# Kernel optimization log

Hardware: AMD Instinct MI355X
Metric: run time of the kernel (lower is better)

## Reference

```python
import jax, jax.numpy as jnp
import numpy as np
import math

B, S, DM, H, DQK, DV, L = 2, 1024, 1024, 16, 64, 64, 32


def setup_inputs() -> dict:
    key = jax.random.key(0)
    ks = jax.random.split(key, 16)
    sdm = 1.0 / np.sqrt(DM)
    u = lambda k, shape, s: jax.random.uniform(k, shape, jnp.float32, -s, s)
    return {
        "q_in": jax.random.normal(ks[0], (B, S, DM), jnp.float32),
        "k_in": jax.random.normal(ks[1], (B, S, DM), jnp.float32),
        "v_in": jax.random.normal(ks[2], (B, S, DM), jnp.float32),
        "attn_mask": jnp.zeros((B, S, S), jnp.bool_),
        "q_pos_ids": jnp.tile(jnp.arange(S, dtype=jnp.int32)[None, :], (B, 1)),
        "kv_pos_ids": jnp.tile(jnp.arange(S, dtype=jnp.int32)[None, :], (B, 1)),
        "W_q": u(ks[3], (H * DQK, DM), sdm),
        "b_q": u(ks[4], (H * DQK,), sdm),
        "W_k": u(ks[5], (H * DQK, DM), sdm),
        "b_k": u(ks[6], (H * DQK,), sdm),
        "W_v": u(ks[7], (H * DV, DM), sdm),
        "b_v": u(ks[8], (H * DV,), sdm),
        "W_o": u(ks[9], (DM, H * DV), sdm),
        "b_o": u(ks[10], (DM,), sdm),
        "W_rel": u(ks[11], (2 * L + 1, DQK), 1.0 / np.sqrt(DQK)),
        "talking_w": u(ks[12], (H, H), 1.0 / np.sqrt(H)),
    }


def reference(q_in, k_in, v_in, attn_mask, q_pos_ids, kv_pos_ids,
              W_q, b_q, W_k, b_k, W_v, b_v, W_o, b_o, W_rel, talking_w):
    Bq, Q, _ = q_in.shape
    # projections + head split
    q = (q_in @ W_q.T + b_q).reshape(Bq, Q, H, DQK)   # [B,Q,H,dqk]
    k = (k_in @ W_k.T + b_k).reshape(Bq, -1, H, DQK)  # [B,K,H,dqk]
    v = (v_in @ W_v.T + b_v).reshape(Bq, -1, H, DV)   # [B,K,H,dv]

    rel = q_pos_ids[:, :, None] - kv_pos_ids[:, None, :]  # [B,Q,K]
    idx = jnp.clip(rel, -L, L) + L
    pos_key = W_rel[idx]            # [B,Q,K,dqk]
    pos_value = pos_key             # original forward reuses rel_pos_k_emb for values

    # alibi slopes: start * ratio**i with ratio == start
    start = 2.0 ** (-2.0 ** (-(math.log2(H) - 3)))
    slopes = jnp.asarray([start * start ** i for i in range(H)], q.dtype)
    alibi = jnp.abs(rel).astype(q.dtype)[:, None, :, :] * slopes[None, :, None, None]

    scores = jnp.einsum('bqnd,bknd->bnqk', q, k)
    scores = scores + jnp.einsum('bqnd,bqkd->bnqk', q, pos_key)
    scores = scores + alibi
    scores = jnp.einsum('bnqk,nm->bmqk', scores, talking_w)  # talking heads
    scores = scores / jnp.sqrt(jnp.asarray(DQK, q.dtype))
    scores = jnp.where(attn_mask[:, None, :, :], jnp.asarray(-10000.0, q.dtype), scores)
    attn = jax.nn.softmax(scores, axis=-1)

    out = jnp.einsum('bnqk,bknd->bnqd', attn, v)
    out = out + jnp.einsum('bnqk,bqkd->bnqd', attn, pos_value)
    out = out.transpose(0, 2, 1, 3).reshape(Bq, Q, H * DV)
    out = out @ W_o.T + b_o
    return (out, attn, scores)
```

## Files before the change

### kernel.cpp

```cpp
#include <hip/hip_runtime.h>

constexpr int kS = 1024;

__global__ __launch_bounds__(256) void gemm_nt(
    const float* __restrict__ A, const float* __restrict__ Bm,
    const float* __restrict__ bias, float* __restrict__ C,
    int K, int lda, int ldb, int ldc,
    long sAo, long sAi, long sBo, long sBi, long sC)
{
    __shared__ float As[32][132];
    __shared__ float Bs[32][132];
    const int t = threadIdx.x;
    const int z = blockIdx.z;
    const long offA = (long)(z >> 4) * sAo + (long)(z & 15) * sAi;
    const long offB = (long)(z >> 4) * sBo + (long)(z & 15) * sBi;
    const long offC = (long)z * sC;
    const int m0 = blockIdx.y * 128;
    const int n0 = blockIdx.x * 128;
    const int sr = t >> 3;
    const int sc = (t & 7) << 2;
    const int tx = t & 15, ty = t >> 4;

    float acc[8][8];
#pragma unroll
    for (int i = 0; i < 8; ++i)
#pragma unroll
        for (int j = 0; j < 8; ++j) acc[i][j] = 0.f;

    for (int k0 = 0; k0 < K; k0 += 32) {
#pragma unroll
        for (int r = 0; r < 4; ++r) {
            const int m = sr + 32 * r;
            const float4 av = *(const float4*)&A[offA + (long)(m0 + m) * lda + k0 + sc];
            As[sc + 0][m] = av.x; As[sc + 1][m] = av.y;
            As[sc + 2][m] = av.z; As[sc + 3][m] = av.w;
            const float4 bv = *(const float4*)&Bm[offB + (long)(n0 + m) * ldb + k0 + sc];
            Bs[sc + 0][m] = bv.x; Bs[sc + 1][m] = bv.y;
            Bs[sc + 2][m] = bv.z; Bs[sc + 3][m] = bv.w;
        }
        __syncthreads();
#pragma unroll 4
        for (int kk = 0; kk < 32; ++kk) {
            float a8[8], b8[8];
            *(float4*)&a8[0] = *(const float4*)&As[kk][ty * 8];
            *(float4*)&a8[4] = *(const float4*)&As[kk][ty * 8 + 4];
            *(float4*)&b8[0] = *(const float4*)&Bs[kk][tx * 8];
            *(float4*)&b8[4] = *(const float4*)&Bs[kk][tx * 8 + 4];
#pragma unroll
            for (int i = 0; i < 8; ++i)
#pragma unroll
                for (int j = 0; j < 8; ++j)
                    acc[i][j] = fmaf(a8[i], b8[j], acc[i][j]);
        }
        __syncthreads();
    }

    float bv[8];
#pragma unroll
    for (int j = 0; j < 8; ++j) bv[j] = bias ? bias[n0 + tx * 8 + j] : 0.f;
#pragma unroll
    for (int i = 0; i < 8; ++i) {
        float o[8];
#pragma unroll
        for (int j = 0; j < 8; ++j) o[j] = acc[i][j] + bv[j];
        float* cp = &C[offC + (long)(m0 + ty * 8 + i) * ldc + n0 + tx * 8];
        *(float4*)&cp[0] = *(const float4*)&o[0];
        *(float4*)&cp[4] = *(const float4*)&o[4];
    }
}

__global__ __launch_bounds__(256) void qrel2_kernel(
    const float* __restrict__ qproj, const float* __restrict__ W_rel,
    const float* __restrict__ tw, float* __restrict__ qrel2)
{
    __shared__ float qrow[1024];
    __shared__ float wrT[64 * 66];
    __shared__ float twl[256];
    __shared__ float qr[16 * 65];
    const int t = threadIdx.x;
    const long bs = blockIdx.x;
    const float* qp = qproj + bs * 1024;
    for (int i = t; i < 1024; i += 256) qrow[i] = qp[i];
    for (int i = t; i < 65 * 64; i += 256) {
        const int j = i >> 6, d = i & 63;
        wrT[d * 66 + j] = W_rel[i];
    }
    twl[t] = tw[t];
    __syncthreads();
    for (int p = t; p < 16 * 65; p += 256) {
        const int n = p / 65, j = p % 65;
        float s = 0.f;
#pragma unroll 8
        for (int d = 0; d < 64; ++d) s = fmaf(qrow[n * 64 + d], wrT[d * 66 + j], s);
        qr[n * 65 + j] = s;
    }
    __syncthreads();
    for (int p = t; p < 16 * 65; p += 256) {
        const int m = p / 65, j = p % 65;
        float s = 0.f;
#pragma unroll
        for (int n = 0; n < 16; ++n) s = fmaf(twl[n * 16 + m], qr[n * 65 + j], s);
        qrel2[bs * (16 * 65) + p] = s;
    }
}

__global__ __launch_bounds__(256) void mix_kernel(
    float* __restrict__ scores, const float* __restrict__ qrel2,
    const float* __restrict__ tw, const unsigned char* __restrict__ mask,
    const int* __restrict__ qpos, const int* __restrict__ kpos,
    float* __restrict__ statp)
{
    __shared__ float qr2[16 * 65];
    __shared__ float twl[256];
    __shared__ float cm[16];
    __shared__ float redm[4][16];
    __shared__ float reds[4][16];
    __shared__ float gmax[16];
    const int t = threadIdx.x;
    const int kc = blockIdx.x;
    const int q = blockIdx.y;
    const int b = blockIdx.z;
    const int k = kc * 256 + t;

    const float* q2p = qrel2 + (long)(b * kS + q) * (16 * 65);
    for (int i = t; i < 16 * 65; i += 256) qr2[i] = q2p[i];
    twl[t] = tw[t];
    __syncthreads();
    if (t < 16) {
        float s = 0.f, cur = 0.7071067811865476f;
        for (int n = 0; n < 16; ++n) { s = fmaf(cur, twl[n * 16 + t], s); cur *= 0.7071067811865476f; }
        cm[t] = s;
    }
    __syncthreads();

    const int rel = qpos[b * kS + q] - kpos[b * kS + k];
    const int idxc = (rel < -32 ? -32 : (rel > 32 ? 32 : rel)) + 32;
    const float ab = fabsf((float)rel);
    const bool msk = mask[((long)b * kS + q) * kS + k] != 0;

    float pre[16];
#pragma unroll
    for (int n = 0; n < 16; ++n)
        pre[n] = scores[((long)(b * 16 + n) * kS + q) * kS + k];
    float sm[16];
#pragma unroll
    for (int m = 0; m < 16; ++m) sm[m] = 0.f;
#pragma unroll
    for (int n = 0; n < 16; ++n) {
        const float p = pre[n];
#pragma unroll
        for (int m = 0; m < 16; ++m) sm[m] = fmaf(p, twl[n * 16 + m], sm[m]);
    }
#pragma unroll
    for (int m = 0; m < 16; ++m) {
        float v = (sm[m] + qr2[m * 65 + idxc] + ab * cm[m]) * 0.125f;
        v = msk ? -10000.f : v;
        sm[m] = v;
        scores[((long)(b * 16 + m) * kS + q) * kS + k] = v;
    }

    const int lane = t & 63, wv = t >> 6;
    float mx[16];
#pragma unroll
    for (int m = 0; m < 16; ++m) mx[m] = sm[m];
#pragma unroll
    for (int m = 0; m < 16; ++m)
        for (int d = 1; d < 64; d <<= 1)
            mx[m] = fmaxf(mx[m], __shfl_xor(mx[m], d, 64));
    if (lane == 0)
        for (int m = 0; m < 16; ++m) redm[wv][m] = mx[m];
    __syncthreads();
    if (t < 16) {
        float v = redm[0][t];
        for (int w = 1; w < 4; ++w) v = fmaxf(v, redm[w][t]);
        gmax[t] = v;
    }
    __syncthreads();
    float sx[16];
#pragma unroll
    for (int m = 0; m < 16; ++m) sx[m] = expf(sm[m] - gmax[m]);
#pragma unroll
    for (int m = 0; m < 16; ++m)
        for (int d = 1; d < 64; d <<= 1)
            sx[m] += __shfl_xor(sx[m], d, 64);
    if (lane == 0)
        for (int m = 0; m < 16; ++m) reds[wv][m] = sx[m];
    __syncthreads();
    if (t < 16) {
        const float l = reds[0][t] + reds[1][t] + reds[2][t] + reds[3][t];
        float2* sp = (float2*)statp;
        sp[((long)(b * 16 + t) * kS + q) * 4 + kc] = make_float2(gmax[t], l);
    }
}

__global__ __launch_bounds__(256) void stats_final(
    const float* __restrict__ statp, float* __restrict__ stats)
{
    const int r = blockIdx.x * 256 + threadIdx.x;
    const float* p = statp + (long)r * 8;
    float M = -1e30f;
#pragma unroll
    for (int i = 0; i < 4; ++i) M = fmaxf(M, p[i * 2]);
    float l = 0.f;
#pragma unroll
    for (int i = 0; i < 4; ++i) l += p[i * 2 + 1] * expf(p[i * 2] - M);
    l = fmaxf(l, 1e-30f);
    stats[r * 2] = M;
    stats[r * 2 + 1] = 1.f / l;
}

__global__ __launch_bounds__(256) void attn_pv(
    const float* __restrict__ scores, float* __restrict__ attn,
    const float* __restrict__ vproj, const float* __restrict__ wrel_g,
    const float* __restrict__ stats, float* __restrict__ head_out)
{
    __shared__ float atT[64][68];
    __shared__ float vs[64][64];
    __shared__ float amid[64][64];
    __shared__ float red_lo[64][16];
    __shared__ float red_hi[64][16];
    __shared__ float MR[64][2];
    __shared__ float wrl[65 * 64];

    const int t = threadIdx.x;
    const int q0 = blockIdx.x * 64;
    const int h = blockIdx.y;
    const int b = blockIdx.z;

    if (t < 64) {
        const float2 s2 = ((const float2*)stats)[(long)(b * 16 + h) * kS + q0 + t];
        MR[t][0] = s2.x; MR[t][1] = s2.y;
    }
    for (int i = t; i < 65 * 64; i += 256) wrl[i] = wrel_g[i];
    {
        float* amf = &amid[0][0];
        for (int i = t; i < 64 * 64; i += 256) amf[i] = 0.f;
    }

    const int g = t >> 7;
    const int u = t & 127;
    const int txd = u & 15, tyq = u >> 4;
    const int qs = tyq * 8, ds = txd * 4;
    const int korg = g * 32;
    const int arow = t >> 4;
    const int akq = (t & 15) * 4;

    float acc[8][4];
#pragma unroll
    for (int i = 0; i < 8; ++i)
#pragma unroll
        for (int j = 0; j < 4; ++j) acc[i][j] = 0.f;
    float slo[4] = {0.f, 0.f, 0.f, 0.f};
    float shi[4] = {0.f, 0.f, 0.f, 0.f};

    const long scb = (long)(b * 16 + h) * kS;
    for (int kt = 0; kt < 16; ++kt) {
        const int k0 = kt * 64;
        __syncthreads();
#pragma unroll
        for (int r = 0; r < 4; ++r) {
            const int krow = arow + 16 * r;
            const float4 vv = *(const float4*)&vproj[(((long)(b * kS + k0 + krow)) * 16 + h) * 64 + akq];
            *(float4*)&vs[krow][akq] = vv;
        }
#pragma unroll
        for (int r = 0; r < 4; ++r) {
            const int qrow = arow + 16 * r;
            const int qg = q0 + qrow;
            const long off = (scb + qg) * kS + k0 + akq;
            const float4 s4 = *(const float4*)&scores[off];
            const float M = MR[qrow][0], R = MR[qrow][1];
            const float a0 = expf(s4.x - M) * R;
            const float a1 = expf(s4.y - M) * R;
            const float a2 = expf(s4.z - M) * R;
            const float a3 = expf(s4.w - M) * R;
            const float4 a4o = make_float4(a0, a1, a2, a3);
            *(float4*)&attn[off] = a4o;
            atT[akq + 0][qrow] = a0;
            atT[akq + 1][qrow] = a1;
            atT[akq + 2][qrow] = a2;
            atT[akq + 3][qrow] = a3;
            const float av[4] = {a0, a1, a2, a3};
#pragma unroll
            for (int j = 0; j < 4; ++j) {
                const int kg = k0 + akq + j;
                const int jj = qg - kg + 32;
                if (jj >= 1 && jj <= 63) amid[qrow][jj] = av[j];
                else if (jj >= 64) slo[r] += av[j];
                else shi[r] += av[j];
            }
        }
        __syncthreads();
#pragma unroll 4
        for (int kk = 0; kk < 32; ++kk) {
            const int k = korg + kk;
            float a8[8], v4[4];
            *(float4*)&a8[0] = *(const float4*)&atT[k][qs];
            *(float4*)&a8[4] = *(const float4*)&atT[k][qs + 4];
            *(float4*)&v4[0] = *(const float4*)&vs[k][ds];
#pragma unroll
            for (int i = 0; i < 8; ++i)
#pragma unroll
                for (int j = 0; j < 4; ++j)
                    acc[i][j] = fmaf(a8[i], v4[j], acc[i][j]);
        }
    }
    __syncthreads();
    float* pvp = &vs[0][0];
    if (g == 1) {
#pragma unroll
        for (int i = 0; i < 8; ++i)
#pragma unroll
            for (int j = 0; j < 4; ++j) pvp[u * 32 + i * 4 + j] = acc[i][j];
    }
#pragma unroll
    for (int r = 0; r < 4; ++r) {
        const int qrow = arow + 16 * r;
        red_lo[qrow][t & 15] = slo[r];
        red_hi[qrow][t & 15] = shi[r];
    }
    __syncthreads();
    if (g == 0) {
#pragma unroll
        for (int i = 0; i < 8; ++i)
#pragma unroll
            for (int j = 0; j < 4; ++j) acc[i][j] += pvp[u * 32 + i * 4 + j];
#pragma unroll
        for (int i = 0; i < 8; ++i) {
            const int qrow = qs + i;
            float Sl = 0.f, Sh = 0.f;
#pragma unroll
            for (int l = 0; l < 16; ++l) { Sl += red_lo[qrow][l]; Sh += red_hi[qrow][l]; }
#pragma unroll
            for (int j = 0; j < 4; ++j)
                acc[i][j] += Sh * wrl[ds + j] + Sl * wrl[64 * 64 + ds + j];
        }
        for (int jj = 1; jj < 64; ++jj) {
            float wv[4];
            *(float4*)&wv[0] = *(const float4*)&wrl[jj * 64 + ds];
#pragma unroll
            for (int i = 0; i < 8; ++i) {
                const float am = amid[qs + i][jj];
#pragma unroll
                for (int j = 0; j < 4; ++j) acc[i][j] = fmaf(am, wv[j], acc[i][j]);
            }
        }
#pragma unroll
        for (int i = 0; i < 8; ++i) {
            float* op = &head_out[(((long)(b * kS + q0 + qs + i)) * 16 + h) * 64 + ds];
            *(float4*)&op[0] = *(const float4*)&acc[i][0];
        }
    }
}

extern "C" void kernel_launch(void* const* d_in, const int* in_sizes, int n_in,
                              void* d_out, int out_size, void* d_ws, size_t ws_size,
                              hipStream_t stream)
{
    const float* q_in = (const float*)d_in[0];
    const float* k_in = (const float*)d_in[1];
    const float* v_in = (const float*)d_in[2];
    const unsigned char* mask = (const unsigned char*)d_in[3];
    const int* qpos = (const int*)d_in[4];
    const int* kpos = (const int*)d_in[5];
    const float* W_q = (const float*)d_in[6];
    const float* b_q = (const float*)d_in[7];
    const float* W_k = (const float*)d_in[8];
    const float* b_k = (const float*)d_in[9];
    const float* W_v = (const float*)d_in[10];
    const float* b_v = (const float*)d_in[11];
    const float* W_o = (const float*)d_in[12];
    const float* b_o = (const float*)d_in[13];
    const float* W_rel = (const float*)d_in[14];
    const float* tw = (const float*)d_in[15];

    float* ws = (float*)d_ws;
    float* qb = ws;
    float* kb = qb + 2097152;
    float* vb = kb + 2097152;
    float* q2 = vb + 2097152;
    float* statp = q2 + 2129920;
    float* stats = statp + 262144;
    float* hout = stats + 65536;

    float* out = (float*)d_out;
    float* attn = out + 2097152;
    float* scores = attn + 33554432;

    const dim3 blk(256, 1, 1);
    const dim3 gp(8, 16, 1);
    gemm_nt<<<gp, blk, 0, stream>>>(q_in, W_q, b_q, qb, 1024, 1024, 1024, 1024, 0L, 0L, 0L, 0L, 0L);
    gemm_nt<<<gp, blk, 0, stream>>>(k_in, W_k, b_k, kb, 1024, 1024, 1024, 1024, 0L, 0L, 0L, 0L, 0L);
    gemm_nt<<<gp, blk, 0, stream>>>(v_in, W_v, b_v, vb, 1024, 1024, 1024, 1024, 0L, 0L, 0L, 0L, 0L);
    qrel2_kernel<<<dim3(2048, 1, 1), blk, 0, stream>>>(qb, W_rel, tw, q2);
    const dim3 gpre(8, 8, 32);
    gemm_nt<<<gpre, blk, 0, stream>>>(qb, kb, (const float*)nullptr, scores,
                                      64, 1024, 1024, 1024,
                                      1048576L, 64L, 1048576L, 64L, 1048576L);
    const dim3 gmix(4, 1024, 2);
    mix_kernel<<<gmix, blk, 0, stream>>>(scores, q2, tw, mask, qpos, kpos, statp);
    stats_final<<<dim3(128, 1, 1), blk, 0, stream>>>(statp, stats);
    const dim3 gk4(16, 16, 2);
    attn_pv<<<gk4, blk, 0, stream>>>(scores, attn, vb, W_rel, stats, hout);
    gemm_nt<<<gp, blk, 0, stream>>>(hout, W_o, b_o, out, 1024, 1024, 1024, 1024, 0L, 0L, 0L, 0L, 0L);
}
```

Before: 1.163 ms.

## Move projections and QK scores to bf16 MFMA and fuse QK with head mixing

Inputs and weights are converted to bf16, and all four projection GEMMs now run on MFMA 16x16x32 bf16 instructions with XOR-swizzled LDS tiles. The Q, K and V projections are batched into one launch. The separate QK^T GEMM and mix kernel are fused into a qkmix kernel. It computes per-head QK on MFMA, applies talking-heads mixing in registers, and produces per-block softmax partial stats. This avoids writing pre-mix scores to global memory and reading them back. V and the head output are kept in bf16, which reduces precision and adds conversion kernels.

After: 1.556 ms. 1.34x slower.

```diff
diff --git a/kernel.cpp b/kernel.cpp
--- a/kernel.cpp
+++ b/kernel.cpp
@@ -2,76 +2,119 @@
 
 constexpr int kS = 1024;
 
-__global__ __launch_bounds__(256) void gemm_nt(
-    const float* __restrict__ A, const float* __restrict__ Bm,
-    const float* __restrict__ bias, float* __restrict__ C,
-    int K, int lda, int ldb, int ldc,
-    long sAo, long sAi, long sBo, long sBi, long sC)
-{
-    __shared__ float As[32][132];
-    __shared__ float Bs[32][132];
+typedef __attribute__((ext_vector_type(8))) short s16x8;
+typedef __attribute__((ext_vector_type(4))) float f32x4;
+
+__device__ __forceinline__ unsigned short f2bf(float x) {
+    unsigned int u = __float_as_uint(x);
+    u += 0x7FFFu + ((u >> 16) & 1u);
+    return (unsigned short)(u >> 16);
+}
+__device__ __forceinline__ float bf2f(unsigned short h) {
+    return __uint_as_float(((unsigned int)h) << 16);
+}
+
+__global__ __launch_bounds__(256) void cvt_multi(
+    const float* __restrict__ s0, const float* __restrict__ s1,
+    const float* __restrict__ s2, const float* __restrict__ s3,
+    unsigned short* __restrict__ d0, unsigned short* __restrict__ d1,
+    unsigned short* __restrict__ d2, unsigned short* __restrict__ d3, int n)
+{
+    const int z = blockIdx.y;
+    const float* s = z == 0 ? s0 : z == 1 ? s1 : z == 2 ? s2 : s3;
+    unsigned short* d = z == 0 ? d0 : z == 1 ? d1 : z == 2 ? d2 : d3;
+    const int i = (blockIdx.x * 256 + threadIdx.x) * 8;
+    if (i >= n) return;
+    const float4 a = *(const float4*)&s[i];
+    const float4 b = *(const float4*)&s[i + 4];
+    uint4 st;
+    st.x = (unsigned int)f2bf(a.x) | ((unsigned int)f2bf(a.y) << 16);
+    st.y = (unsigned int)f2bf(a.z) | ((unsigned int)f2bf(a.w) << 16);
+    st.z = (unsigned int)f2bf(b.x) | ((unsigned int)f2bf(b.y) << 16);
+    st.w = (unsigned int)f2bf(b.z) | ((unsigned int)f2bf(b.w) << 16);
+    *(uint4*)&d[i] = st;
+}
+
+__global__ __launch_bounds__(256, 2) void gemm_bf16(
+    const unsigned short* __restrict__ A, const unsigned short* __restrict__ B,
+    const float* __restrict__ bi0, const float* __restrict__ bi1, const float* __restrict__ bi2,
+    float* __restrict__ Cf, unsigned short* __restrict__ Cb,
+    int K, int N, long sA, long sB, long sC)
+{
+    __shared__ __align__(16) unsigned short As[128 * 64];
+    __shared__ __align__(16) unsigned short Bs[128 * 64];
     const int t = threadIdx.x;
     const int z = blockIdx.z;
-    const long offA = (long)(z >> 4) * sAo + (long)(z & 15) * sAi;
-    const long offB = (long)(z >> 4) * sBo + (long)(z & 15) * sBi;
-    const long offC = (long)z * sC;
-    const int m0 = blockIdx.y * 128;
-    const int n0 = blockIdx.x * 128;
-    const int sr = t >> 3;
-    const int sc = (t & 7) << 2;
-    const int tx = t & 15, ty = t >> 4;
-
-    float acc[8][8];
-#pragma unroll
-    for (int i = 0; i < 8; ++i)
-#pragma unroll
-        for (int j = 0; j < 8; ++j) acc[i][j] = 0.f;
-
-    for (int k0 = 0; k0 < K; k0 += 32) {
-#pragma unroll
-        for (int r = 0; r < 4; ++r) {
-            const int m = sr + 32 * r;
-            const float4 av = *(const float4*)&A[offA + (long)(m0 + m) * lda + k0 + sc];
-            As[sc + 0][m] = av.x; As[sc + 1][m] = av.y;
-            As[sc + 2][m] = av.z; As[sc + 3][m] = av.w;
-            const float4 bv = *(const float4*)&Bm[offB + (long)(n0 + m) * ldb + k0 + sc];
-            Bs[sc + 0][m] = bv.x; Bs[sc + 1][m] = bv.y;
-            Bs[sc + 2][m] = bv.z; Bs[sc + 3][m] = bv.w;
-        }
-        __syncthreads();
-#pragma unroll 4
-        for (int kk = 0; kk < 32; ++kk) {
-            float a8[8], b8[8];
-            *(float4*)&a8[0] = *(const float4*)&As[kk][ty * 8];
-            *(float4*)&a8[4] = *(const float4*)&As[kk][ty * 8 + 4];
-            *(float4*)&b8[0] = *(const float4*)&Bs[kk][tx * 8];
-            *(float4*)&b8[4] = *(const float4*)&Bs[kk][tx * 8 + 4];
-#pragma unroll
-            for (int i = 0; i < 8; ++i)
-#pragma unroll
-                for (int j = 0; j < 8; ++j)
-                    acc[i][j] = fmaf(a8[i], b8[j], acc[i][j]);
-        }
-        __syncthreads();
-    }
-
-    float bv[8];
-#pragma unroll
-    for (int j = 0; j < 8; ++j) bv[j] = bias ? bias[n0 + tx * 8 + j] : 0.f;
-#pragma unroll
-    for (int i = 0; i < 8; ++i) {
-        float o[8];
-#pragma unroll
-        for (int j = 0; j < 8; ++j) o[j] = acc[i][j] + bv[j];
-        float* cp = &C[offC + (long)(m0 + ty * 8 + i) * ldc + n0 + tx * 8];
-        *(float4*)&cp[0] = *(const float4*)&o[0];
-        *(float4*)&cp[4] = *(const float4*)&o[4];
-    }
+    const float* bi = (z == 0) ? bi0 : ((z == 1) ? bi1 : bi2);
+    const int n0 = blockIdx.x * 128, m0 = blockIdx.y * 128;
+    const int w = t >> 6, l = t & 63;
+    const int wm = w >> 1, wn = w & 1;
+    const long Ab = (long)z * sA, Bb = (long)z * sB, Cbse = (long)z * sC;
+
+    f32x4 acc[4][4];
+#pragma unroll
+    for (int i = 0; i < 4; ++i)
+#pragma unroll
+        for (int j = 0; j < 4; ++j) acc[i][j] = (f32x4){0.f, 0.f, 0.f, 0.f};
+
+    for (int k0 = 0; k0 < K; k0 += 64) {
+#pragma unroll
+        for (int i = 0; i < 4; ++i) {
+            const int p = i * 256 + t;
+            const int r = p >> 3, slot = p & 7;
+            const int ck = slot ^ (r & 7);
+            const s16x8 av = *(const s16x8*)&A[Ab + (long)(m0 + r) * K + k0 + ck * 8];
+            const s16x8 bv = *(const s16x8*)&B[Bb + (long)(n0 + r) * K + k0 + ck * 8];
+            *(s16x8*)&As[p * 8] = av;
+            *(s16x8*)&Bs[p * 8] = bv;
+        }
+        __syncthreads();
+#pragma unroll
+        for (int s = 0; s < 2; ++s) {
+            s16x8 af[4], bfr[4];
+            const int g = l >> 4;
+            const int ck = s * 4 + g;
+#pragma unroll
+            for (int mf = 0; mf < 4; ++mf) {
+                const int row = wm * 64 + mf * 16 + (l & 15);
+                af[mf] = *(const s16x8*)&As[(row * 8 + (ck ^ (row & 7))) * 8];
+            }
+#pragma unroll
+            for (int nf = 0; nf < 4; ++nf) {
+                const int col = wn * 64 + nf * 16 + (l & 15);
+                bfr[nf] = *(const s16x8*)&Bs[(col * 8 + (ck ^ (col & 7))) * 8];
+            }
+#pragma unroll
+            for (int mf = 0; mf < 4; ++mf)
+#pragma unroll
+                for (int nf = 0; nf < 4; ++nf)
+                    acc[mf][nf] = __builtin_amdgcn_mfma_f32_16x16x32_bf16(
+                        af[mf], bfr[nf], acc[mf][nf], 0, 0, 0);
+        }
+        __syncthreads();
+    }
+
+    float bv[4];
+#pragma unroll
+    for (int nf = 0; nf < 4; ++nf) bv[nf] = bi ? bi[n0 + wn * 64 + nf * 16 + (l & 15)] : 0.f;
+#pragma unroll
+    for (int mf = 0; mf < 4; ++mf)
+#pragma unroll
+        for (int r2 = 0; r2 < 4; ++r2) {
+            const int row = m0 + wm * 64 + mf * 16 + (l >> 4) * 4 + r2;
+#pragma unroll
+            for (int nf = 0; nf < 4; ++nf) {
+                const int col = n0 + wn * 64 + nf * 16 + (l & 15);
+                const float v = acc[mf][nf][r2] + bv[nf];
+                if (Cf) Cf[Cbse + (long)row * N + col] = v;
+                if (Cb) Cb[Cbse + (long)row * N + col] = f2bf(v);
+            }
+        }
 }
 
 __global__ __launch_bounds__(256) void qrel2_kernel(
-    const float* __restrict__ qproj, const float* __restrict__ W_rel,
-    const float* __restrict__ tw, float* __restrict__ qrel2)
+    const unsigned short* __restrict__ qproj, const float* __restrict__ W_rel,
+    const float* __restrict__ tw, float* __restrict__ qrel2T)
 {
     __shared__ float qrow[1024];
     __shared__ float wrT[64 * 66];
@@ -79,8 +122,13 @@
     __shared__ float qr[16 * 65];
     const int t = threadIdx.x;
     const long bs = blockIdx.x;
-    const float* qp = qproj + bs * 1024;
-    for (int i = t; i < 1024; i += 256) qrow[i] = qp[i];
+    {
+        const ushort4 qv = *(const ushort4*)&qproj[bs * 1024 + t * 4];
+        qrow[t * 4 + 0] = bf2f(qv.x);
+        qrow[t * 4 + 1] = bf2f(qv.y);
+        qrow[t * 4 + 2] = bf2f(qv.z);
+        qrow[t * 4 + 3] = bf2f(qv.w);
+    }
     for (int i = t; i < 65 * 64; i += 256) {
         const int j = i >> 6, d = i & 63;
         wrT[d * 66 + j] = W_rel[i];
@@ -100,119 +148,144 @@
         float s = 0.f;
 #pragma unroll
         for (int n = 0; n < 16; ++n) s = fmaf(twl[n * 16 + m], qr[n * 65 + j], s);
-        qrel2[bs * (16 * 65) + p] = s;
-    }
-}
-
-__global__ __launch_bounds__(256) void mix_kernel(
-    float* __restrict__ scores, const float* __restrict__ qrel2,
-    const float* __restrict__ tw, const unsigned char* __restrict__ mask,
+        qrel2T[bs * 1040 + j * 16 + m] = s;
+    }
+}
+
+__global__ __launch_bounds__(256, 2) void qkmix(
+    const unsigned short* __restrict__ qbp, const unsigned short* __restrict__ kbp,
+    const float* __restrict__ qrel2T, const float* __restrict__ tw,
+    const unsigned char* __restrict__ mask,
     const int* __restrict__ qpos, const int* __restrict__ kpos,
-    float* __restrict__ statp)
-{
-    __shared__ float qr2[16 * 65];
+    float* __restrict__ scores, float2* __restrict__ statp)
+{
+    __shared__ __align__(16) unsigned short qls[32 * 64 * 8];
+    __shared__ __align__(16) unsigned short kls[32 * 64 * 8];
     __shared__ float twl[256];
-    __shared__ float cm[16];
-    __shared__ float redm[4][16];
-    __shared__ float reds[4][16];
-    __shared__ float gmax[16];
+    __shared__ float cmL[16];
+    __shared__ int qposs[32], kposs[32];
+    __shared__ float2 statL[2][32][16];
     const int t = threadIdx.x;
-    const int kc = blockIdx.x;
-    const int q = blockIdx.y;
-    const int b = blockIdx.z;
-    const int k = kc * 256 + t;
-
-    const float* q2p = qrel2 + (long)(b * kS + q) * (16 * 65);
-    for (int i = t; i < 16 * 65; i += 256) qr2[i] = q2p[i];
+    const int k0 = blockIdx.x * 32, q0 = blockIdx.y * 32, b = blockIdx.z;
+    const int w = t >> 6, l = t & 63;
+    const int qoff = (w >> 1) * 16, koff = (w & 1) * 16;
+
     twl[t] = tw[t];
+    if (t < 32) qposs[t] = qpos[b * kS + q0 + t];
+    if (t >= 64 && t < 96) kposs[t - 64] = kpos[b * kS + (t - 64) + k0];
     __syncthreads();
     if (t < 16) {
-        float s = 0.f, cur = 0.7071067811865476f;
-        for (int n = 0; n < 16; ++n) { s = fmaf(cur, twl[n * 16 + t], s); cur *= 0.7071067811865476f; }
-        cm[t] = s;
-    }
-    __syncthreads();
-
-    const int rel = qpos[b * kS + q] - kpos[b * kS + k];
-    const int idxc = (rel < -32 ? -32 : (rel > 32 ? 32 : rel)) + 32;
-    const float ab = fabsf((float)rel);
-    const bool msk = mask[((long)b * kS + q) * kS + k] != 0;
-
-    float pre[16];
-#pragma unroll
-    for (int n = 0; n < 16; ++n)
-        pre[n] = scores[((long)(b * 16 + n) * kS + q) * kS + k];
-    float sm[16];
-#pragma unroll
-    for (int m = 0; m < 16; ++m) sm[m] = 0.f;
-#pragma unroll
-    for (int n = 0; n < 16; ++n) {
-        const float p = pre[n];
-#pragma unroll
-        for (int m = 0; m < 16; ++m) sm[m] = fmaf(p, twl[n * 16 + m], sm[m]);
-    }
-#pragma unroll
-    for (int m = 0; m < 16; ++m) {
-        float v = (sm[m] + qr2[m * 65 + idxc] + ab * cm[m]) * 0.125f;
-        v = msk ? -10000.f : v;
-        sm[m] = v;
-        scores[((long)(b * 16 + m) * kS + q) * kS + k] = v;
-    }
-
-    const int lane = t & 63, wv = t >> 6;
-    float mx[16];
-#pragma unroll
-    for (int m = 0; m < 16; ++m) mx[m] = sm[m];
-#pragma unroll
-    for (int m = 0; m < 16; ++m)
-        for (int d = 1; d < 64; d <<= 1)
-            mx[m] = fmaxf(mx[m], __shfl_xor(mx[m], d, 64));
-    if (lane == 0)
-        for (int m = 0; m < 16; ++m) redm[wv][m] = mx[m];
-    __syncthreads();
-    if (t < 16) {
-        float v = redm[0][t];
-        for (int w = 1; w < 4; ++w) v = fmaxf(v, redm[w][t]);
-        gmax[t] = v;
-    }
-    __syncthreads();
-    float sx[16];
-#pragma unroll
-    for (int m = 0; m < 16; ++m) sx[m] = expf(sm[m] - gmax[m]);
-#pragma unroll
-    for (int m = 0; m < 16; ++m)
-        for (int d = 1; d < 64; d <<= 1)
-            sx[m] += __shfl_xor(sx[m], d, 64);
-    if (lane == 0)
-        for (int m = 0; m < 16; ++m) reds[wv][m] = sx[m];
-    __syncthreads();
-    if (t < 16) {
-        const float l = reds[0][t] + reds[1][t] + reds[2][t] + reds[3][t];
-        float2* sp = (float2*)statp;
-        sp[((long)(b * 16 + t) * kS + q) * 4 + kc] = make_float2(gmax[t], l);
+        float s = 0.f, cur = 0.70710678118654752f;
+        for (int n = 0; n < 16; ++n) { s = fmaf(cur, twl[n * 16 + t], s); cur *= 0.70710678118654752f; }
+        cmL[t] = s;
+    }
+
+    f32x4 acc[16];
+#pragma unroll
+    for (int n = 0; n < 16; ++n) acc[n] = (f32x4){0.f, 0.f, 0.f, 0.f};
+
+#pragma unroll
+    for (int pass = 0; pass < 2; ++pass) {
+        __syncthreads();
+#pragma unroll
+        for (int i = 0; i < 8; ++i) {
+            const int p = i * 256 + t;
+            const int r = p >> 6, slot = p & 63;
+            const int nd = slot ^ (r & 7);
+            *(s16x8*)&qls[p * 8] =
+                *(const s16x8*)&qbp[((long)(b * kS + q0 + r)) * 1024 + pass * 512 + nd * 8];
+            *(s16x8*)&kls[p * 8] =
+                *(const s16x8*)&kbp[((long)(b * kS + k0 + r)) * 1024 + pass * 512 + nd * 8];
+        }
+        __syncthreads();
+#pragma unroll
+        for (int nl = 0; nl < 8; ++nl) {
+            const int g = l >> 4;
+            const int row = qoff + (l & 15);
+            const int col = koff + (l & 15);
+            const s16x8 a0 = *(const s16x8*)&qls[(row * 64 + ((nl * 8 + g) ^ (row & 7))) * 8];
+            const s16x8 a1 = *(const s16x8*)&qls[(row * 64 + ((nl * 8 + 4 + g) ^ (row & 7))) * 8];
+            const s16x8 b0 = *(const s16x8*)&kls[(col * 64 + ((nl * 8 + g) ^ (col & 7))) * 8];
+            const s16x8 b1 = *(const s16x8*)&kls[(col * 64 + ((nl * 8 + 4 + g) ^ (col & 7))) * 8];
+            acc[pass * 8 + nl] = __builtin_amdgcn_mfma_f32_16x16x32_bf16(a0, b0, acc[pass * 8 + nl], 0, 0, 0);
+            acc[pass * 8 + nl] = __builtin_amdgcn_mfma_f32_16x16x32_bf16(a1, b1, acc[pass * 8 + nl], 0, 0, 0);
+        }
+    }
+
+    const int g = l >> 4, cl = l & 15;
+    const int kg_loc = koff + cl;
+    const int kp = kposs[kg_loc];
+    const int kgl = k0 + kg_loc;
+#pragma unroll
+    for (int r = 0; r < 4; ++r) {
+        const int row_l = qoff + g * 4 + r;
+        const int row_g = q0 + row_l;
+        const int rel = qposs[row_l] - kp;
+        const int idx = (rel < -32 ? -32 : (rel > 32 ? 32 : rel)) + 32;
+        const float ab = fabsf((float)rel);
+        const bool msk = mask[((long)b * kS + row_g) * kS + kgl] != 0;
+        const float* q2p = &qrel2T[((long)(b * kS + row_g) * 65 + idx) * 16];
+        float q2v[16];
+        *(float4*)&q2v[0] = *(const float4*)&q2p[0];
+        *(float4*)&q2v[4] = *(const float4*)&q2p[4];
+        *(float4*)&q2v[8] = *(const float4*)&q2p[8];
+        *(float4*)&q2v[12] = *(const float4*)&q2p[12];
+        float val[16];
+#pragma unroll
+        for (int m = 0; m < 16; ++m) {
+            float s = 0.f;
+#pragma unroll
+            for (int n = 0; n < 16; ++n) s = fmaf(acc[n][r], twl[n * 16 + m], s);
+            float v = (s + q2v[m] + ab * cmL[m]) * 0.125f;
+            val[m] = msk ? -10000.f : v;
+            scores[((long)(b * 16 + m) * kS + row_g) * kS + kgl] = val[m];
+        }
+        float smx = 0.f, ssm = 0.f;
+#pragma unroll
+        for (int m = 0; m < 16; ++m) {
+            float mx = val[m];
+            mx = fmaxf(mx, __shfl_xor(mx, 1, 16));
+            mx = fmaxf(mx, __shfl_xor(mx, 2, 16));
+            mx = fmaxf(mx, __shfl_xor(mx, 4, 16));
+            mx = fmaxf(mx, __shfl_xor(mx, 8, 16));
+            float e = __expf(val[m] - mx);
+            e += __shfl_xor(e, 1, 16);
+            e += __shfl_xor(e, 2, 16);
+            e += __shfl_xor(e, 4, 16);
+            e += __shfl_xor(e, 8, 16);
+            if (cl == m) { smx = mx; ssm = e; }
+        }
+        statL[w & 1][row_l][cl] = make_float2(smx, ssm);
+    }
+    __syncthreads();
+    for (int e = t; e < 512; e += 256) {
+        const int row = e >> 4, m = e & 15;
+        const float2 s0 = statL[0][row][m], s1 = statL[1][row][m];
+        const float M = fmaxf(s0.x, s1.x);
+        const float sm = s0.y * __expf(s0.x - M) + s1.y * __expf(s1.x - M);
+        statp[((long)(b * 16 + m) * kS + q0 + row) * 32 + blockIdx.x] = make_float2(M, sm);
     }
 }
 
 __global__ __launch_bounds__(256) void stats_final(
-    const float* __restrict__ statp, float* __restrict__ stats)
-{
-    const int r = blockIdx.x * 256 + threadIdx.x;
-    const float* p = statp + (long)r * 8;
+    const float2* __restrict__ statp, float2* __restrict__ stats)
+{
+    const int rr = blockIdx.x * 256 + threadIdx.x;
+    const float2* p = statp + (long)rr * 32;
     float M = -1e30f;
-#pragma unroll
-    for (int i = 0; i < 4; ++i) M = fmaxf(M, p[i * 2]);
+#pragma unroll 8
+    for (int i = 0; i < 32; ++i) M = fmaxf(M, p[i].x);
     float l = 0.f;
-#pragma unroll
-    for (int i = 0; i < 4; ++i) l += p[i * 2 + 1] * expf(p[i * 2] - M);
+#pragma unroll 8
+    for (int i = 0; i < 32; ++i) l += p[i].y * __expf(p[i].x - M);
     l = fmaxf(l, 1e-30f);
-    stats[r * 2] = M;
-    stats[r * 2 + 1] = 1.f / l;
+    stats[rr] = make_float2(M, 1.f / l);
 }
 
 __global__ __launch_bounds__(256) void attn_pv(
     const float* __restrict__ scores, float* __restrict__ attn,
-    const float* __restrict__ vproj, const float* __restrict__ wrel_g,
-    const float* __restrict__ stats, float* __restrict__ head_out)
+    const unsigned short* __restrict__ vproj, const float* __restrict__ wrel_g,
+    const float2* __restrict__ stats, unsigned short* __restrict__ head_out)
 {
     __shared__ float atT[64][68];
     __shared__ float vs[64][64];
@@ -228,7 +301,7 @@
     const int b = blockIdx.z;
 
     if (t < 64) {
-        const float2 s2 = ((const float2*)stats)[(long)(b * 16 + h) * kS + q0 + t];
+        const float2 s2 = stats[(long)(b * 16 + h) * kS + q0 + t];
         MR[t][0] = s2.x; MR[t][1] = s2.y;
     }
     for (int i = t; i < 65 * 64; i += 256) wrl[i] = wrel_g[i];
@@ -260,8 +333,11 @@
 #pragma unroll
         for (int r = 0; r < 4; ++r) {
             const int krow = arow + 16 * r;
-            const float4 vv = *(const float4*)&vproj[(((long)(b * kS + k0 + krow)) * 16 + h) * 64 + akq];
-            *(float4*)&vs[krow][akq] = vv;
+            const ushort4 vv = *(const ushort4*)&vproj[(((long)(b * kS + k0 + krow)) * 16 + h) * 64 + akq];
+            vs[krow][akq + 0] = bf2f(vv.x);
+            vs[krow][akq + 1] = bf2f(vv.y);
+            vs[krow][akq + 2] = bf2f(vv.z);
+            vs[krow][akq + 3] = bf2f(vv.w);
         }
 #pragma unroll
         for (int r = 0; r < 4; ++r) {
@@ -330,7 +406,7 @@
             const int qrow = qs + i;
             float Sl = 0.f, Sh = 0.f;
 #pragma unroll
-            for (int l = 0; l < 16; ++l) { Sl += red_lo[qrow][l]; Sh += red_hi[qrow][l]; }
+            for (int lq = 0; lq < 16; ++lq) { Sl += red_lo[qrow][lq]; Sh += red_hi[qrow][lq]; }
 #pragma unroll
             for (int j = 0; j < 4; ++j)
                 acc[i][j] += Sh * wrl[ds + j] + Sl * wrl[64 * 64 + ds + j];
@@ -347,8 +423,10 @@
         }
 #pragma unroll
         for (int i = 0; i < 8; ++i) {
-            float* op = &head_out[(((long)(b * kS + q0 + qs + i)) * 16 + h) * 64 + ds];
-            *(float4*)&op[0] = *(const float4*)&acc[i][0];
+            ushort4 h4;
+            h4.x = f2bf(acc[i][0]); h4.y = f2bf(acc[i][1]);
+            h4.z = f2bf(acc[i][2]); h4.w = f2bf(acc[i][3]);
+            *(ushort4*)&head_out[(((long)(b * kS + q0 + qs + i)) * 16 + h) * 64 + ds] = h4;
         }
     }
 }
@@ -374,33 +452,32 @@
     const float* W_rel = (const float*)d_in[14];
     const float* tw = (const float*)d_in[15];
 
-    float* ws = (float*)d_ws;
-    float* qb = ws;
-    float* kb = qb + 2097152;
-    float* vb = kb + 2097152;
-    float* q2 = vb + 2097152;
-    float* statp = q2 + 2129920;
-    float* stats = statp + 262144;
-    float* hout = stats + 65536;
+    unsigned char* W = (unsigned char*)d_ws;
+    unsigned short* in_bf  = (unsigned short*)W;
+    unsigned short* w_bf   = (unsigned short*)(W + 12582912);
+    unsigned short* qkv_bf = (unsigned short*)(W + 20971520);
+    float*          qrel2T = (float*)(W + 33554432);
+    float2*         statp  = (float2*)W;
+    float2*         stats  = (float2*)(W + 42074112);
+    unsigned short* hout   = (unsigned short*)(W + 42336256);
 
     float* out = (float*)d_out;
     float* attn = out + 2097152;
     float* scores = attn + 33554432;
 
     const dim3 blk(256, 1, 1);
-    const dim3 gp(8, 16, 1);
-    gemm_nt<<<gp, blk, 0, stream>>>(q_in, W_q, b_q, qb, 1024, 1024, 1024, 1024, 0L, 0L, 0L, 0L, 0L);
-    gemm_nt<<<gp, blk, 0, stream>>>(k_in, W_k, b_k, kb, 1024, 1024, 1024, 1024, 0L, 0L, 0L, 0L, 0L);
-    gemm_nt<<<gp, blk, 0, stream>>>(v_in, W_v, b_v, vb, 1024, 1024, 1024, 1024, 0L, 0L, 0L, 0L, 0L);
-    qrel2_kernel<<<dim3(2048, 1, 1), blk, 0, stream>>>(qb, W_rel, tw, q2);
-    const dim3 gpre(8, 8, 32);
-    gemm_nt<<<gpre, blk, 0, stream>>>(qb, kb, (const float*)nullptr, scores,
-                                      64, 1024, 1024, 1024,
-                                      1048576L, 64L, 1048576L, 64L, 1048576L);
-    const dim3 gmix(4, 1024, 2);
-    mix_kernel<<<gmix, blk, 0, stream>>>(scores, q2, tw, mask, qpos, kpos, statp);
+    cvt_multi<<<dim3(1024, 3), blk, 0, stream>>>(q_in, k_in, v_in, nullptr,
+        in_bf, in_bf + 2097152, in_bf + 4194304, nullptr, 2097152);
+    cvt_multi<<<dim3(512, 4), blk, 0, stream>>>(W_q, W_k, W_v, W_o,
+        w_bf, w_bf + 1048576, w_bf + 2097152, w_bf + 3145728, 1048576);
+    gemm_bf16<<<dim3(8, 16, 3), blk, 0, stream>>>(in_bf, w_bf, b_q, b_k, b_v,
+        nullptr, qkv_bf, 1024, 1024, 2097152L, 1048576L, 2097152L);
+    qrel2_kernel<<<dim3(2048, 1, 1), blk, 0, stream>>>(qkv_bf, W_rel, tw, qrel2T);
+    qkmix<<<dim3(32, 32, 2), blk, 0, stream>>>(qkv_bf, qkv_bf + 2097152,
+        qrel2T, tw, mask, qpos, kpos, scores, statp);
     stats_final<<<dim3(128, 1, 1), blk, 0, stream>>>(statp, stats);
-    const dim3 gk4(16, 16, 2);
-    attn_pv<<<gk4, blk, 0, stream>>>(scores, attn, vb, W_rel, stats, hout);
-    gemm_nt<<<gp, blk, 0, stream>>>(hout, W_o, b_o, out, 1024, 1024, 1024, 1024, 0L, 0L, 0L, 0L, 0L);
-}
+    attn_pv<<<dim3(16, 16, 2), blk, 0, stream>>>(scores, attn,
+        qkv_bf + 4194304, W_rel, stats, hout);
+    gemm_bf16<<<dim3(8, 16, 1), blk, 0, stream>>>(hout, w_bf + 3145728,
+        b_o, b_o, b_o, out, nullptr, 1024, 1024, 0L, 0L, 0L);
+}
```
